# Optimization experiments

Hardware: AMD Instinct MI355X
Metric: run time of the kernel (lower is better)

The kernel has to match this reference:

```python
import jax, jax.numpy as jnp
import numpy as np

D_MODEL = 1024
N_EXPERTS = 8
CAPACITY = 2048


def setup_inputs() -> dict:
    key = jax.random.key(0)
    ks = jax.random.split(key, 8)
    D, E, H = D_MODEL, N_EXPERTS, 4 * D_MODEL
    s = lambda fan_in: 1.0 / np.sqrt(fan_in)
    return {
        "x": jax.random.normal(ks[0], (4, 2048, D), dtype=jnp.float32),
        "Wg": jax.random.uniform(ks[1], (D, E), minval=-s(D), maxval=s(D)),
        "bg": jax.random.uniform(ks[2], (E,), minval=-s(D), maxval=s(D)),
        "W1": jax.random.uniform(ks[3], (E, D, H), minval=-s(D), maxval=s(D)),
        "b1": jax.random.uniform(ks[4], (E, H), minval=-s(D), maxval=s(D)),
        "W2": jax.random.uniform(ks[5], (E, H, D), minval=-s(H), maxval=s(H)),
        "b2": jax.random.uniform(ks[6], (E, D), minval=-s(H), maxval=s(H)),
        "top_k": 1,
    }


def reference(x, Wg, bg, W1, b1, W2, b2, top_k):
    B, S, D = x.shape
    E, C = N_EXPERTS, CAPACITY
    x_flat = x.reshape(-1, D)                      # [N, D]
    N = x_flat.shape[0]

    # Router: top-k expert indices per token
    logits = x_flat @ Wg + bg                      # [N, E]
    _, routes = jax.lax.top_k(logits, top_k)       # [N, k]
    r = routes.reshape(-1)                         # [N*k] row-major, matches torch flatten order
    tok = jnp.repeat(jnp.arange(N), top_k)         # token id per routing slot

    # Position of each routed token within its expert's queue (arrival order)
    oh = (r[:, None] == jnp.arange(E)[None, :]).astype(jnp.int32)  # [N*k, E]
    pos = jnp.cumsum(oh, axis=0)[jnp.arange(r.shape[0]), r] - 1    # [N*k]
    kept = pos < C
    slot = jnp.where(kept, pos, C)                 # dropped tokens -> overflow slot C

    # Dispatch: gather tokens into per-expert padded buffers [E, C, D]
    disp = jnp.zeros((E, C + 1, D), dtype=x.dtype).at[r, slot].set(x_flat[tok])
    disp = disp[:, :C]

    # Per-expert MLP (grouped GEMMs)
    h = jax.nn.relu(jnp.einsum('ecd,edh->ech', disp, W1) + b1[:, None, :])
    y = jnp.einsum('ech,ehd->ecd', h, W2) + b2[:, None, :]  # [E, C, D]

    # Combine: scatter expert outputs back; dropped tokens stay zero
    gathered = y[r, jnp.minimum(pos, C - 1)]       # [N*k, D]
    out_flat = jnp.zeros((N, D), dtype=x.dtype).at[tok].set(
        jnp.where(kept[:, None], gathered, 0.0))
    return out_flat.reshape(B, S, D)
```

## Files before the change

### kernel.cpp

```cpp
#include <hip/hip_runtime.h>


#define N_TOK   8192
#define DMODEL  1024
#define HDIM    4096
#define NEXP    8
#define CAP     2048
#define MAXROWS 9216

typedef float  f32x4  __attribute__((ext_vector_type(4)));
typedef __bf16 bf16x8 __attribute__((ext_vector_type(8)));

typedef void __attribute__((address_space(1))) as1_void;
typedef void __attribute__((address_space(3))) as3_void;

__device__ __forceinline__ void async_copy16(void* lds, const void* g) {
    __builtin_amdgcn_global_load_lds((as1_void*)g, (as3_void*)lds, 16, 0, 0);
}

__device__ __forceinline__ unsigned short f2bf(float f) {
    unsigned u = __float_as_uint(f);
    unsigned r = (u + 0x7fffu + ((u >> 16) & 1u)) >> 16;
    return (unsigned short)r;
}

__global__ __launch_bounds__(256) void gate_kernel(
    const float* __restrict__ x, const float* __restrict__ Wg,
    const float* __restrict__ bg, int* __restrict__ route)
{
    const int wave = threadIdx.x >> 6, lane = threadIdx.x & 63;
    const int tok = blockIdx.x * 4 + wave;
    const float* xr = x + (size_t)tok * DMODEL;
    double acc[8];
#pragma unroll
    for (int e = 0; e < 8; ++e) acc[e] = 0.0;
    for (int i = 0; i < DMODEL / 64; ++i) {
        const int d = i * 64 + lane;
        const double xv = (double)xr[d];
        const float* wr = Wg + (size_t)d * 8;
#pragma unroll
        for (int e = 0; e < 8; ++e) acc[e] += xv * (double)wr[e];
    }
#pragma unroll
    for (int e = 0; e < 8; ++e) {
        double v = acc[e];
#pragma unroll
        for (int off = 32; off > 0; off >>= 1) v += __shfl_down(v, off, 64);
        acc[e] = v;
    }
    if (lane == 0) {
        double bv = acc[0] + (double)bg[0];
        int bi = 0;
#pragma unroll
        for (int e = 1; e < 8; ++e) {
            double v = acc[e] + (double)bg[e];
            if (v > bv) { bv = v; bi = e; }
        }
        route[tok] = bi;
    }
}

__global__ __launch_bounds__(256) void scan_kernel(
    const int* __restrict__ route, int* __restrict__ tokrow,
    int* __restrict__ meta)
{
    __shared__ int hist[256][8];
    __shared__ int cntS[8];
    __shared__ int rowbaseS[8];
    const int tid = threadIdx.x;
    for (int i = tid; i < MAXROWS; i += 256) tokrow[i] = -1;
    const int t0 = tid * 32;
    int r[32];
#pragma unroll
    for (int i = 0; i < 32; ++i) r[i] = route[t0 + i];
    int loc[8];
#pragma unroll
    for (int e = 0; e < 8; ++e) loc[e] = 0;
#pragma unroll
    for (int i = 0; i < 32; ++i) {
#pragma unroll
        for (int e = 0; e < 8; ++e) loc[e] += (r[i] == e) ? 1 : 0;
    }
#pragma unroll
    for (int e = 0; e < 8; ++e) hist[tid][e] = loc[e];
    __syncthreads();
    if (tid < 8) {
        int run = 0;
        for (int t = 0; t < 256; ++t) { int v = hist[t][tid]; hist[t][tid] = run; run += v; }
        meta[tid] = run;
        cntS[tid] = run;
    }
    __syncthreads();
    if (tid == 0) {
        int rb = 0;
#pragma unroll
        for (int e = 0; e < 8; ++e) {
            int c = cntS[e]; if (c > CAP) c = CAP;
            int p = (c + 127) & ~127;
            meta[8 + e] = p;
            meta[16 + e] = rb;
            rowbaseS[e] = rb;
            rb += p;
        }
        meta[24] = rb;
    }
    __syncthreads();
    int base[8];
#pragma unroll
    for (int e = 0; e < 8; ++e) base[e] = hist[tid][e];
#pragma unroll
    for (int i = 0; i < 32; ++i) {
        const int e = r[i];
        const int p = base[e]++;
        if (p < CAP) tokrow[rowbaseS[e] + p] = t0 + i;
    }
}

__global__ __launch_bounds__(256) void dispatch_kernel(
    const float* __restrict__ x, const int* __restrict__ tokrow,
    unsigned short* __restrict__ xg)
{
    const int row = blockIdx.x;
    const int tok = tokrow[row];
    const int d = threadIdx.x * 4;
    float4 v = make_float4(0.f, 0.f, 0.f, 0.f);
    if (tok >= 0) v = *(const float4*)(x + (size_t)tok * DMODEL + d);
    ushort4 o;
    o.x = f2bf(v.x); o.y = f2bf(v.y); o.z = f2bf(v.z); o.w = f2bf(v.w);
    *(ushort4*)(xg + (size_t)row * DMODEL + d) = o;
}

__global__ void transpose_cast_kernel(const float* __restrict__ in,
                                      unsigned short* __restrict__ out,
                                      int R, int C)
{
    __shared__ float t[32][33];
    const size_t base = (size_t)blockIdx.z * R * C;
    const int c0 = blockIdx.x * 32, r0 = blockIdx.y * 32;
    const int x = threadIdx.x, y0 = threadIdx.y;
#pragma unroll
    for (int i = 0; i < 4; ++i) {
        int y = y0 + i * 8;
        t[y][x] = in[base + (size_t)(r0 + y) * C + c0 + x];
    }
    __syncthreads();
#pragma unroll
    for (int i = 0; i < 4; ++i) {
        int y = y0 + i * 8;
        out[base + (size_t)(c0 + y) * R + r0 + x] = f2bf(t[x][y]);
    }
}

__device__ __forceinline__ void mfma_mainloop(
    const unsigned short* __restrict__ A,
    const unsigned short* __restrict__ B,
    int K, int tid, f32x4 acc[4][4])
{
    __shared__ __align__(16) char smem[16384];
    const int wave = tid >> 6, lane = tid & 63;
    const int mrow = lane >> 2;
    const int kofs = (lane & 3) * 8;
    const int quad = lane >> 4, l16 = lane & 15;
    const int wm = (wave & 1) * 64, wn = (wave >> 1) * 64;

    for (int k0 = 0; k0 < K; k0 += 32) {
        __syncthreads();
#pragma unroll
        for (int i = 0; i < 2; ++i) {
            const int m = wave * 32 + i * 16 + mrow;
            async_copy16(smem + wave * 2048 + i * 1024 + lane * 16,
                         A + (size_t)m * K + k0 + kofs);
        }
#pragma unroll
        for (int i = 0; i < 2; ++i) {
            const int n = wave * 32 + i * 16 + mrow;
            async_copy16(smem + 8192 + wave * 2048 + i * 1024 + lane * 16,
                         B + (size_t)n * K + k0 + kofs);
        }
        __syncthreads();
        bf16x8 a[4], b[4];
#pragma unroll
        for (int mi = 0; mi < 4; ++mi)
            a[mi] = *(const bf16x8*)(smem + ((wm + mi * 16 + l16) * 32 + quad * 8) * 2);
#pragma unroll
        for (int ni = 0; ni < 4; ++ni)
            b[ni] = *(const bf16x8*)(smem + 8192 + ((wn + ni * 16 + l16) * 32 + quad * 8) * 2);
#pragma unroll
        for (int mi = 0; mi < 4; ++mi)
#pragma unroll
            for (int ni = 0; ni < 4; ++ni)
                acc[mi][ni] = __builtin_amdgcn_mfma_f32_16x16x32_bf16(
                    a[mi], b[ni], acc[mi][ni], 0, 0, 0);
    }
}

__global__ __launch_bounds__(256) void gemm1_kernel(
    const unsigned short* __restrict__ xg,
    const unsigned short* __restrict__ wb,
    const float* __restrict__ b1,
    unsigned short* __restrict__ hbuf,
    const int* __restrict__ meta)
{
    const int e = blockIdx.z, mtile = blockIdx.y, ntile = blockIdx.x;
    if (mtile * 128 >= meta[8 + e]) return;
    const int row0 = meta[16 + e] + mtile * 128;
    const int tid = threadIdx.x;

    f32x4 acc[4][4];
#pragma unroll
    for (int mi = 0; mi < 4; ++mi)
#pragma unroll
        for (int ni = 0; ni < 4; ++ni)
#pragma unroll
            for (int r = 0; r < 4; ++r) acc[mi][ni][r] = 0.0f;

    mfma_mainloop(xg + (size_t)row0 * DMODEL,
                  wb + ((size_t)e * HDIM + (size_t)ntile * 128) * DMODEL,
                  DMODEL, tid, acc);

    __shared__ __align__(16) unsigned short hl[128 * 128];
    const int wave = tid >> 6, lane = tid & 63;
    const int quad = lane >> 4, l16 = lane & 15;
    const int wm = (wave & 1) * 64, wn = (wave >> 1) * 64;
    const float* bias = b1 + (size_t)e * HDIM + (size_t)ntile * 128;
#pragma unroll
    for (int mi = 0; mi < 4; ++mi)
#pragma unroll
        for (int ni = 0; ni < 4; ++ni) {
            const int cc = wn + ni * 16 + l16;
            const float bv = bias[cc];
#pragma unroll
            for (int r = 0; r < 4; ++r) {
                const int rr = wm + mi * 16 + quad * 4 + r;
                hl[rr * 128 + cc] = f2bf(fmaxf(acc[mi][ni][r] + bv, 0.0f));
            }
        }
    __syncthreads();
#pragma unroll
    for (int i = 0; i < 8; ++i) {
        const int c = tid + i * 256;
        const int m = c >> 4;
        const int nb = (c & 15) * 8;
        *(int4*)(hbuf + (size_t)(row0 + m) * HDIM + (size_t)ntile * 128 + nb) =
            *(const int4*)(hl + m * 128 + nb);
    }
}

__global__ __launch_bounds__(256) void gemm2_kernel(
    const unsigned short* __restrict__ hbuf,
    const unsigned short* __restrict__ wb,
    const float* __restrict__ b2,
    const int* __restrict__ tokrow,
    float* __restrict__ out,
    const int* __restrict__ meta)
{
    const int e = blockIdx.z, mtile = blockIdx.y, ntile = blockIdx.x;
    if (mtile * 128 >= meta[8 + e]) return;
    const int row0 = meta[16 + e] + mtile * 128;
    const int tid = threadIdx.x;

    f32x4 acc[4][4];
#pragma unroll
    for (int mi = 0; mi < 4; ++mi)
#pragma unroll
        for (int ni = 0; ni < 4; ++ni)
#pragma unroll
            for (int r = 0; r < 4; ++r) acc[mi][ni][r] = 0.0f;

    mfma_mainloop(hbuf + (size_t)row0 * HDIM,
                  wb + ((size_t)e * DMODEL + (size_t)ntile * 128) * HDIM,
                  HDIM, tid, acc);

    const int wave = tid >> 6, lane = tid & 63;
    const int quad = lane >> 4, l16 = lane & 15;
    const int wm = (wave & 1) * 64, wn = (wave >> 1) * 64;
#pragma unroll
    for (int mi = 0; mi < 4; ++mi) {
#pragma unroll
        for (int r = 0; r < 4; ++r) {
            const int rowl = wm + mi * 16 + quad * 4 + r;
            const int tok = tokrow[row0 + rowl];
            if (tok >= 0) {
#pragma unroll
                for (int ni = 0; ni < 4; ++ni) {
                    const int col = ntile * 128 + wn + ni * 16 + l16;
                    out[(size_t)tok * DMODEL + col] =
                        acc[mi][ni][r] + b2[(size_t)e * DMODEL + col];
                }
            }
        }
    }
}

extern "C" void kernel_launch(void* const* d_in, const int* in_sizes, int n_in,
                              void* d_out, int out_size, void* d_ws, size_t ws_size,
                              hipStream_t stream) {
    (void)in_sizes; (void)n_in; (void)out_size; (void)ws_size;
    const float* x  = (const float*)d_in[0];
    const float* Wg = (const float*)d_in[1];
    const float* bg = (const float*)d_in[2];
    const float* W1 = (const float*)d_in[3];
    const float* b1 = (const float*)d_in[4];
    const float* W2 = (const float*)d_in[5];
    const float* b2 = (const float*)d_in[6];
    float* out = (float*)d_out;
    char* ws = (char*)d_ws;

    int* route  = (int*)ws;
    int* tokrow = (int*)(ws + 32768);
    int* meta   = (int*)(ws + 69632);
    unsigned short* xg   = (unsigned short*)(ws + (size_t)131072);
    unsigned short* hbuf = (unsigned short*)(ws + (size_t)20 * 1024 * 1024);
    unsigned short* wb   = (unsigned short*)(ws + (size_t)96 * 1024 * 1024);

    hipMemsetAsync(d_out, 0, (size_t)N_TOK * DMODEL * sizeof(float), stream);

    gate_kernel<<<N_TOK / 4, 256, 0, stream>>>(x, Wg, bg, route);
    scan_kernel<<<1, 256, 0, stream>>>(route, tokrow, meta);
    dispatch_kernel<<<MAXROWS, 256, 0, stream>>>(x, tokrow, xg);

    transpose_cast_kernel<<<dim3(HDIM / 32, DMODEL / 32, NEXP), dim3(32, 8), 0, stream>>>(
        W1, wb, DMODEL, HDIM);
    gemm1_kernel<<<dim3(HDIM / 128, 16, NEXP), 256, 0, stream>>>(
        xg, wb, b1, hbuf, meta);

    transpose_cast_kernel<<<dim3(DMODEL / 32, HDIM / 32, NEXP), dim3(32, 8), 0, stream>>>(
        W2, wb, HDIM, DMODEL);
    gemm2_kernel<<<dim3(DMODEL / 128, 16, NEXP), 256, 0, stream>>>(
        hbuf, wb, b2, tokrow, out, meta);
}
```

Before: 592.3 us.

## Split-K second expert GEMM with reduction pass; widen transpose-cast stores; share LDS

The second grouped GEMM is split in two along K when the workspace is large enough. Slice 0 writes bias plus partial sum straight to the output and slice 1 writes partials to a float buffer, which a new reduce kernel adds in. This doubles the block count to fill more CUs for the long K=4096 loop. The cost is an extra 36 MB partial write and read plus one more launch. The transpose-cast kernel now handles 64 rows per block and stores bf16 pairs, and gemm1 reuses one LDS buffer for the mainloop and the epilogue.

```diff
diff --git a/kernel.cpp b/kernel.cpp
--- a/kernel.cpp
+++ b/kernel.cpp
@@ -134,48 +134,50 @@
                                       unsigned short* __restrict__ out,
                                       int R, int C)
 {
-    __shared__ float t[32][33];
+    __shared__ float t[64][33];
     const size_t base = (size_t)blockIdx.z * R * C;
-    const int c0 = blockIdx.x * 32, r0 = blockIdx.y * 32;
+    const int c0 = blockIdx.x * 32, r0 = blockIdx.y * 64;
     const int x = threadIdx.x, y0 = threadIdx.y;
 #pragma unroll
+    for (int i = 0; i < 8; ++i) {
+        const int r = y0 + i * 8;
+        t[r][x] = in[base + (size_t)(r0 + r) * C + c0 + x];
+    }
+    __syncthreads();
+#pragma unroll
     for (int i = 0; i < 4; ++i) {
-        int y = y0 + i * 8;
-        t[y][x] = in[base + (size_t)(r0 + y) * C + c0 + x];
-    }
-    __syncthreads();
-#pragma unroll
-    for (int i = 0; i < 4; ++i) {
-        int y = y0 + i * 8;
-        out[base + (size_t)(c0 + y) * R + r0 + x] = f2bf(t[x][y]);
+        const int c = y0 + i * 8;
+        ushort2 o;
+        o.x = f2bf(t[2 * x][c]);
+        o.y = f2bf(t[2 * x + 1][c]);
+        *(ushort2*)(&out[base + (size_t)(c0 + c) * R + r0 + 2 * x]) = o;
     }
 }
 
 __device__ __forceinline__ void mfma_mainloop(
     const unsigned short* __restrict__ A,
     const unsigned short* __restrict__ B,
-    int K, int tid, f32x4 acc[4][4])
-{
-    __shared__ __align__(16) char smem[16384];
+    int ld, int Kiter, int tid, char* smem, f32x4 acc[4][4])
+{
     const int wave = tid >> 6, lane = tid & 63;
     const int mrow = lane >> 2;
     const int kofs = (lane & 3) * 8;
     const int quad = lane >> 4, l16 = lane & 15;
     const int wm = (wave & 1) * 64, wn = (wave >> 1) * 64;
 
-    for (int k0 = 0; k0 < K; k0 += 32) {
+    for (int k0 = 0; k0 < Kiter; k0 += 32) {
         __syncthreads();
 #pragma unroll
         for (int i = 0; i < 2; ++i) {
             const int m = wave * 32 + i * 16 + mrow;
             async_copy16(smem + wave * 2048 + i * 1024 + lane * 16,
-                         A + (size_t)m * K + k0 + kofs);
+                         A + (size_t)m * ld + k0 + kofs);
         }
 #pragma unroll
         for (int i = 0; i < 2; ++i) {
             const int n = wave * 32 + i * 16 + mrow;
             async_copy16(smem + 8192 + wave * 2048 + i * 1024 + lane * 16,
-                         B + (size_t)n * K + k0 + kofs);
+                         B + (size_t)n * ld + k0 + kofs);
         }
         __syncthreads();
         bf16x8 a[4], b[4];
@@ -206,6 +208,8 @@
     const int row0 = meta[16 + e] + mtile * 128;
     const int tid = threadIdx.x;
 
+    __shared__ __align__(16) char lds[32768];
+
     f32x4 acc[4][4];
 #pragma unroll
     for (int mi = 0; mi < 4; ++mi)
@@ -216,9 +220,10 @@
 
     mfma_mainloop(xg + (size_t)row0 * DMODEL,
                   wb + ((size_t)e * HDIM + (size_t)ntile * 128) * DMODEL,
-                  DMODEL, tid, acc);
-
-    __shared__ __align__(16) unsigned short hl[128 * 128];
+                  DMODEL, DMODEL, tid, lds, acc);
+
+    __syncthreads();
+    unsigned short* hl = (unsigned short*)lds;
     const int wave = tid >> 6, lane = tid & 63;
     const int quad = lane >> 4, l16 = lane & 15;
     const int wm = (wave & 1) * 64, wn = (wave >> 1) * 64;
@@ -252,12 +257,19 @@
     const float* __restrict__ b2,
     const int* __restrict__ tokrow,
     float* __restrict__ out,
-    const int* __restrict__ meta)
-{
-    const int e = blockIdx.z, mtile = blockIdx.y, ntile = blockIdx.x;
+    const int* __restrict__ meta,
+    float* __restrict__ pbuf,
+    int sh)
+{
+    const int e = blockIdx.z >> sh;
+    const int s = blockIdx.z & ((1 << sh) - 1);
+    const int mtile = blockIdx.y, ntile = blockIdx.x;
     if (mtile * 128 >= meta[8 + e]) return;
     const int row0 = meta[16 + e] + mtile * 128;
     const int tid = threadIdx.x;
+    const int Ks = HDIM >> sh;
+
+    __shared__ __align__(16) char lds[16384];
 
     f32x4 acc[4][4];
 #pragma unroll
@@ -267,9 +279,9 @@
 #pragma unroll
             for (int r = 0; r < 4; ++r) acc[mi][ni][r] = 0.0f;
 
-    mfma_mainloop(hbuf + (size_t)row0 * HDIM,
-                  wb + ((size_t)e * DMODEL + (size_t)ntile * 128) * HDIM,
-                  HDIM, tid, acc);
+    mfma_mainloop(hbuf + (size_t)row0 * HDIM + (size_t)s * Ks,
+                  wb + ((size_t)e * DMODEL + (size_t)ntile * 128) * HDIM + (size_t)s * Ks,
+                  HDIM, Ks, tid, lds, acc);
 
     const int wave = tid >> 6, lane = tid & 63;
     const int quad = lane >> 4, l16 = lane & 15;
@@ -281,21 +293,43 @@
             const int rowl = wm + mi * 16 + quad * 4 + r;
             const int tok = tokrow[row0 + rowl];
             if (tok >= 0) {
-#pragma unroll
-                for (int ni = 0; ni < 4; ++ni) {
-                    const int col = ntile * 128 + wn + ni * 16 + l16;
-                    out[(size_t)tok * DMODEL + col] =
-                        acc[mi][ni][r] + b2[(size_t)e * DMODEL + col];
+                if (s == 0) {
+#pragma unroll
+                    for (int ni = 0; ni < 4; ++ni) {
+                        const int col = ntile * 128 + wn + ni * 16 + l16;
+                        out[(size_t)tok * DMODEL + col] =
+                            acc[mi][ni][r] + b2[(size_t)e * DMODEL + col];
+                    }
+                } else {
+#pragma unroll
+                    for (int ni = 0; ni < 4; ++ni) {
+                        const int col = ntile * 128 + wn + ni * 16 + l16;
+                        pbuf[(size_t)(row0 + rowl) * DMODEL + col] = acc[mi][ni][r];
+                    }
                 }
             }
         }
     }
+}
+
+__global__ __launch_bounds__(256) void reduce_kernel(
+    const float* __restrict__ pbuf, const int* __restrict__ tokrow,
+    float* __restrict__ out)
+{
+    const int row = blockIdx.x;
+    const int tok = tokrow[row];
+    if (tok < 0) return;
+    const int d = threadIdx.x * 4;
+    f32x4 p = *(const f32x4*)(pbuf + (size_t)row * DMODEL + d);
+    f32x4 o = *(f32x4*)(out + (size_t)tok * DMODEL + d);
+    o += p;
+    *(f32x4*)(out + (size_t)tok * DMODEL + d) = o;
 }
 
 extern "C" void kernel_launch(void* const* d_in, const int* in_sizes, int n_in,
                               void* d_out, int out_size, void* d_ws, size_t ws_size,
                               hipStream_t stream) {
-    (void)in_sizes; (void)n_in; (void)out_size; (void)ws_size;
+    (void)in_sizes; (void)n_in; (void)out_size;
     const float* x  = (const float*)d_in[0];
     const float* Wg = (const float*)d_in[1];
     const float* bg = (const float*)d_in[2];
@@ -312,6 +346,11 @@
     unsigned short* xg   = (unsigned short*)(ws + (size_t)131072);
     unsigned short* hbuf = (unsigned short*)(ws + (size_t)20 * 1024 * 1024);
     unsigned short* wb   = (unsigned short*)(ws + (size_t)96 * 1024 * 1024);
+    float* pbuf = (float*)(ws + (size_t)160 * 1024 * 1024);
+
+    const size_t splitk_need = (size_t)160 * 1024 * 1024
+                             + (size_t)MAXROWS * DMODEL * sizeof(float);
+    const bool use_splitk = (ws_size >= splitk_need);
 
     hipMemsetAsync(d_out, 0, (size_t)N_TOK * DMODEL * sizeof(float), stream);
 
@@ -319,13 +358,20 @@
     scan_kernel<<<1, 256, 0, stream>>>(route, tokrow, meta);
     dispatch_kernel<<<MAXROWS, 256, 0, stream>>>(x, tokrow, xg);
 
-    transpose_cast_kernel<<<dim3(HDIM / 32, DMODEL / 32, NEXP), dim3(32, 8), 0, stream>>>(
+    transpose_cast_kernel<<<dim3(HDIM / 32, DMODEL / 64, NEXP), dim3(32, 8), 0, stream>>>(
         W1, wb, DMODEL, HDIM);
     gemm1_kernel<<<dim3(HDIM / 128, 16, NEXP), 256, 0, stream>>>(
         xg, wb, b1, hbuf, meta);
 
-    transpose_cast_kernel<<<dim3(DMODEL / 32, HDIM / 32, NEXP), dim3(32, 8), 0, stream>>>(
+    transpose_cast_kernel<<<dim3(DMODEL / 32, HDIM / 64, NEXP), dim3(32, 8), 0, stream>>>(
         W2, wb, HDIM, DMODEL);
-    gemm2_kernel<<<dim3(DMODEL / 128, 16, NEXP), 256, 0, stream>>>(
-        hbuf, wb, b2, tokrow, out, meta);
-}
+
+    if (use_splitk) {
+        gemm2_kernel<<<dim3(DMODEL / 128, 16, NEXP * 2), 256, 0, stream>>>(
+            hbuf, wb, b2, tokrow, out, meta, pbuf, 1);
+        reduce_kernel<<<MAXROWS, 256, 0, stream>>>(pbuf, tokrow, out);
+    } else {
+        gemm2_kernel<<<dim3(DMODEL / 128, 16, NEXP), 256, 0, stream>>>(
+            hbuf, wb, b2, tokrow, out, meta, (float*)nullptr, 0);
+    }
+}
```

Result: slower. 621.7 us (+5.0%).

## Widen transpose-cast tiles, share GEMM LDS, and remap blocks to spread experts across XCDs

Applied to the files above, without the earlier changes.

The weight transpose-cast now handles 128x32 tiles per block and writes four bf16 values per store, so output writes are wider. The GEMM kernels take a caller-provided LDS buffer. GEMM1 reuses the mainloop staging area for its epilogue tile, cutting its LDS footprint from 48KB to 32KB, which may allow more blocks per CU. Block indices are remapped so that consecutive blocks, which round-robin across XCDs, handle the same expert's tiles on the same XCD, aiming for better L2 reuse of weights. The remap adds index arithmetic, and the larger transpose tile reduces the number of transpose blocks.

```diff
diff --git a/kernel.cpp b/kernel.cpp
--- a/kernel.cpp
+++ b/kernel.cpp
@@ -130,33 +130,37 @@
     *(ushort4*)(xg + (size_t)row * DMODEL + d) = o;
 }
 
-__global__ void transpose_cast_kernel(const float* __restrict__ in,
-                                      unsigned short* __restrict__ out,
-                                      int R, int C)
-{
-    __shared__ float t[32][33];
+__global__ __launch_bounds__(256) void transpose_cast_kernel(
+    const float* __restrict__ in, unsigned short* __restrict__ out,
+    int R, int C)
+{
+    __shared__ float t[128][33];
     const size_t base = (size_t)blockIdx.z * R * C;
-    const int c0 = blockIdx.x * 32, r0 = blockIdx.y * 32;
+    const int c0 = blockIdx.x * 32, r0 = blockIdx.y * 128;
     const int x = threadIdx.x, y0 = threadIdx.y;
 #pragma unroll
-    for (int i = 0; i < 4; ++i) {
-        int y = y0 + i * 8;
-        t[y][x] = in[base + (size_t)(r0 + y) * C + c0 + x];
-    }
-    __syncthreads();
-#pragma unroll
-    for (int i = 0; i < 4; ++i) {
-        int y = y0 + i * 8;
-        out[base + (size_t)(c0 + y) * R + r0 + x] = f2bf(t[x][y]);
+    for (int i = 0; i < 16; ++i) {
+        const int r = y0 + i * 8;
+        t[r][x] = in[base + (size_t)(r0 + r) * C + c0 + x];
+    }
+    __syncthreads();
+#pragma unroll
+    for (int j = 0; j < 4; ++j) {
+        const int c = y0 + j * 8;
+        ushort4 o;
+        o.x = f2bf(t[4 * x + 0][c]);
+        o.y = f2bf(t[4 * x + 1][c]);
+        o.z = f2bf(t[4 * x + 2][c]);
+        o.w = f2bf(t[4 * x + 3][c]);
+        *(ushort4*)(&out[base + (size_t)(c0 + c) * R + r0 + 4 * x]) = o;
     }
 }
 
 __device__ __forceinline__ void mfma_mainloop(
     const unsigned short* __restrict__ A,
     const unsigned short* __restrict__ B,
-    int K, int tid, f32x4 acc[4][4])
-{
-    __shared__ __align__(16) char smem[16384];
+    int K, int tid, char* smem, f32x4 acc[4][4])
+{
     const int wave = tid >> 6, lane = tid & 63;
     const int mrow = lane >> 2;
     const int kofs = (lane & 3) * 8;
@@ -201,11 +205,17 @@
     unsigned short* __restrict__ hbuf,
     const int* __restrict__ meta)
 {
-    const int e = blockIdx.z, mtile = blockIdx.y, ntile = blockIdx.x;
+    const int lin = blockIdx.x + 32 * (blockIdx.y + 16 * blockIdx.z);
+    const int work = (lin & 7) * 512 + (lin >> 3);
+    const int e = work >> 9;
+    const int rem = work & 511;
+    const int mtile = rem & 15, ntile = rem >> 4;
     if (mtile * 128 >= meta[8 + e]) return;
     const int row0 = meta[16 + e] + mtile * 128;
     const int tid = threadIdx.x;
 
+    __shared__ __align__(16) char lds[32768];
+
     f32x4 acc[4][4];
 #pragma unroll
     for (int mi = 0; mi < 4; ++mi)
@@ -216,9 +226,10 @@
 
     mfma_mainloop(xg + (size_t)row0 * DMODEL,
                   wb + ((size_t)e * HDIM + (size_t)ntile * 128) * DMODEL,
-                  DMODEL, tid, acc);
-
-    __shared__ __align__(16) unsigned short hl[128 * 128];
+                  DMODEL, tid, lds, acc);
+
+    __syncthreads();
+    unsigned short* hl = (unsigned short*)lds;
     const int wave = tid >> 6, lane = tid & 63;
     const int quad = lane >> 4, l16 = lane & 15;
     const int wm = (wave & 1) * 64, wn = (wave >> 1) * 64;
@@ -254,11 +265,17 @@
     float* __restrict__ out,
     const int* __restrict__ meta)
 {
-    const int e = blockIdx.z, mtile = blockIdx.y, ntile = blockIdx.x;
+    const int lin = blockIdx.x + 8 * (blockIdx.y + 16 * blockIdx.z);
+    const int work = (lin & 7) * 128 + (lin >> 3);
+    const int e = work >> 7;
+    const int rem = work & 127;
+    const int mtile = rem & 15, ntile = rem >> 4;
     if (mtile * 128 >= meta[8 + e]) return;
     const int row0 = meta[16 + e] + mtile * 128;
     const int tid = threadIdx.x;
 
+    __shared__ __align__(16) char lds[16384];
+
     f32x4 acc[4][4];
 #pragma unroll
     for (int mi = 0; mi < 4; ++mi)
@@ -269,7 +286,7 @@
 
     mfma_mainloop(hbuf + (size_t)row0 * HDIM,
                   wb + ((size_t)e * DMODEL + (size_t)ntile * 128) * HDIM,
-                  HDIM, tid, acc);
+                  HDIM, tid, lds, acc);
 
     const int wave = tid >> 6, lane = tid & 63;
     const int quad = lane >> 4, l16 = lane & 15;
@@ -319,12 +336,12 @@
     scan_kernel<<<1, 256, 0, stream>>>(route, tokrow, meta);
     dispatch_kernel<<<MAXROWS, 256, 0, stream>>>(x, tokrow, xg);
 
-    transpose_cast_kernel<<<dim3(HDIM / 32, DMODEL / 32, NEXP), dim3(32, 8), 0, stream>>>(
+    transpose_cast_kernel<<<dim3(HDIM / 32, DMODEL / 128, NEXP), dim3(32, 8), 0, stream>>>(
         W1, wb, DMODEL, HDIM);
     gemm1_kernel<<<dim3(HDIM / 128, 16, NEXP), 256, 0, stream>>>(
         xg, wb, b1, hbuf, meta);
 
-    transpose_cast_kernel<<<dim3(DMODEL / 32, HDIM / 32, NEXP), dim3(32, 8), 0, stream>>>(
+    transpose_cast_kernel<<<dim3(DMODEL / 32, HDIM / 128, NEXP), dim3(32, 8), 0, stream>>>(
         W2, wb, HDIM, DMODEL);
     gemm2_kernel<<<dim3(DMODEL / 128, 16, NEXP), 256, 0, stream>>>(
         hbuf, wb, b2, tokrow, out, meta);
```

New measurement: 581.1 us. No clear change (-1.9%).
